# Optimization experiments

Measured on AMD Instinct MI355X. Metric: run time of the kernel, lower is better.

Reference implementation:

```python
import jax, jax.numpy as jnp
import numpy as np

B, E, C = 128, 16, 128   # batch, n experts (program tokens), module_dim
H = W = 64               # input image size
PROJ, FC, NANS = 512, 1024, 2


def conv2d(x, w, b, padding=1):
    # x: [N,C,H,W], w: [O,I,kh,kw]
    y = jax.lax.conv_general_dilated(
        x, w, (1, 1), [(padding, padding), (padding, padding)],
        dimension_numbers=('NCHW', 'OIHW', 'NCHW'))
    return y + b[None, :, None, None]


def maxpool2(x):
    return jax.lax.reduce_window(x, -jnp.inf, jax.lax.max, (1, 1, 2, 2), (1, 1, 2, 2), 'VALID')


def setup_inputs() -> dict:
    key = jax.random.key(0)
    ks = jax.random.split(key, 12)
    def init(k, shape, fan_in):
        return jax.random.normal(k, shape, jnp.float32) * np.float32(1.0 / np.sqrt(fan_in))
    inp = {}
    inp['image'] = jax.random.normal(ks[0], (B, 3, H, W), jnp.float32)
    inp['question'] = jax.random.randint(ks[1], (B, 8), 0, E)
    # stem: conv3x3 3->C, relu, maxpool2, conv3x3 C->C, relu, maxpool2
    inp['stem_w1'] = init(ks[2], (C, 3, 3, 3), 3 * 9)
    inp['stem_b1'] = jnp.zeros((C,), jnp.float32)
    inp['stem_w2'] = init(ks[3], (C, C, 3, 3), C * 9)
    inp['stem_b2'] = jnp.zeros((C,), jnp.float32)
    # E expert residual blocks, each: conv3x3 C->C, relu, conv3x3 C->C, +res, relu
    inp['exp_w1'] = init(ks[4], (E, C, C, 3, 3), C * 9)
    inp['exp_b1'] = jnp.zeros((E, C), jnp.float32)
    inp['exp_w2'] = init(ks[5], (E, C, C, 3, 3), C * 9)
    inp['exp_b2'] = jnp.zeros((E, C), jnp.float32)
    # classifier: 1x1 conv C->PROJ, relu, maxpool2, flatten, fc->FC, relu, fc->NANS
    inp['proj_w'] = init(ks[6], (PROJ, C, 1, 1), C)
    inp['proj_b'] = jnp.zeros((PROJ,), jnp.float32)
    inp['fc1_w'] = init(ks[7], (FC, PROJ * 8 * 8), PROJ * 8 * 8)
    inp['fc1_b'] = jnp.zeros((FC,), jnp.float32)
    inp['fc2_w'] = init(ks[8], (NANS, FC), FC)
    inp['fc2_b'] = jnp.zeros((NANS,), jnp.float32)
    return inp


def reference(image, question, stem_w1, stem_b1, stem_w2, stem_b2,
              exp_w1, exp_b1, exp_w2, exp_b2,
              proj_w, proj_b, fc1_w, fc1_b, fc2_w, fc2_b):
    # stem -> [B, C, 16, 16]
    h = maxpool2(jax.nn.relu(conv2d(image, stem_w1, stem_b1)))
    h = maxpool2(jax.nn.relu(conv2d(h, stem_w2, stem_b2)))

    def block(x, w1, b1, w2, b2):
        # per-sample residual block with per-sample expert weights; x: [C,h,w]
        x4 = x[None]
        out = jax.nn.relu(conv2d(x4, w1, b1))
        out = conv2d(out, w2, b2)
        return jax.nn.relu(x4 + out)[0]

    # dispatch order matches [color_lhs, lhs, color_rhs, rhs, rel] = cols 3,4,6,7,5
    for col in (3, 4, 6, 7, 5):
        idx = question[:, col]
        h = jax.vmap(block)(h, exp_w1[idx], exp_b1[idx], exp_w2[idx], exp_b2[idx])

    # classifier
    p = maxpool2(jax.nn.relu(conv2d(h, proj_w, proj_b, padding=0)))  # [B,PROJ,8,8]
    f = p.reshape(p.shape[0], -1)
    f = jax.nn.relu(f @ fc1_w.T + fc1_b)
    return f @ fc2_w.T + fc2_b
```

## Files before the change

### kernel.cpp

```cpp
#include <hip/hip_runtime.h>
#include <hip/hip_bf16.h>
#include <cstdint>
#include <cstddef>


typedef __bf16 bf16_t;
typedef __attribute__((ext_vector_type(4))) bf16_t bf16x4;
typedef __attribute__((ext_vector_type(8))) bf16_t bf16x8;
typedef __attribute__((ext_vector_type(16))) float f32x16;
typedef __attribute__((ext_vector_type(4))) float f32x4;

__global__ __launch_bounds__(256) void prep_stem1_k(
    const float* __restrict__ exp_w1, const float* __restrict__ exp_w2,
    const float* __restrict__ stem_w2, const float* __restrict__ proj_w,
    bf16_t* __restrict__ wT1, bf16_t* __restrict__ wT2,
    bf16_t* __restrict__ wTs2, bf16_t* __restrict__ pwT,
    const float* __restrict__ img, const float* __restrict__ w1,
    const float* __restrict__ b1, bf16_t* __restrict__ s1out,
    const float* __restrict__ fc1_w, bf16_t* __restrict__ wbf)
{
  alignas(16) __shared__ char smem[37120];
  int bid = blockIdx.x;
  const int tid = threadIdx.x;

  if (bid >= 2376) {
    const size_t base0 = (size_t)(bid - 2376) * 16384 + (size_t)tid * 8;
#pragma unroll
    for (int it = 0; it < 8; ++it) {
      const size_t idx = base0 + (size_t)it * 2048;
      f32x4 u0 = *(const f32x4*)(fc1_w + idx);
      f32x4 u1 = *(const f32x4*)(fc1_w + idx + 4);
      bf16x8 v;
#pragma unroll
      for (int j = 0; j < 4; ++j) { v[j] = (bf16_t)u0[j]; v[4 + j] = (bf16_t)u1[j]; }
      *(bf16x8*)(wbf + idx) = v;
    }
    return;
  }

  if (bid >= 328) {
    bid -= 328;
    float* sImg = (float*)smem;
    char*  sOut = smem + 4112;
    const int b = bid >> 4, t = bid & 15;
    const int ty0p = (t >> 2) * 8, tx0p = (t & 3) * 8;
    const int lane = tid & 63;
    const int wvbase = __builtin_amdgcn_readfirstlane(tid >> 6) * 32;

    for (int s = tid; s < 972; s += 256) {
      const int ic = s / 324, r2 = s - ic * 324;
      const int rr = r2 / 18, cc = r2 - rr * 18;
      const int gy = 2 * ty0p - 1 + rr, gx = 2 * tx0p - 1 + cc;
      float v = 0.f;
      if (gy >= 0 && gy < 64 && gx >= 0 && gx < 64)
        v = img[(((size_t)b * 3 + ic) * 64 + gy) * 64 + gx];
      sImg[ic * 342 + rr * 19 + cc] = v;
    }
    __syncthreads();

    const int ppy = lane >> 3, ppx = lane & 7;
    const int swz = (lane & 15) << 3;
    char* orow = sOut + lane * 256;

    for (int oc8 = 0; oc8 < 32; oc8 += 8) {
      float acc[8][2][2];
#pragma unroll
      for (int q = 0; q < 8; ++q) {
        const float bv = b1[wvbase + oc8 + q];
#pragma unroll
        for (int i = 0; i < 2; ++i)
#pragma unroll
          for (int jj = 0; jj < 2; ++jj) acc[q][i][jj] = bv;
      }
#pragma unroll
      for (int ic = 0; ic < 3; ++ic)
#pragma unroll
        for (int dy = 0; dy < 3; ++dy)
#pragma unroll
          for (int dx = 0; dx < 3; ++dx) {
            const float p00 = sImg[ic * 342 + (2 * ppy + dy) * 19 + 2 * ppx + dx];
            const float p01 = sImg[ic * 342 + (2 * ppy + dy) * 19 + 2 * ppx + dx + 1];
            const float p10 = sImg[ic * 342 + (2 * ppy + dy + 1) * 19 + 2 * ppx + dx];
            const float p11 = sImg[ic * 342 + (2 * ppy + dy + 1) * 19 + 2 * ppx + dx + 1];
#pragma unroll
            for (int q = 0; q < 8; ++q) {
              const float wv2 = w1[(wvbase + oc8 + q) * 27 + ic * 9 + dy * 3 + dx];
              acc[q][0][0] = fmaf(p00, wv2, acc[q][0][0]);
              acc[q][0][1] = fmaf(p01, wv2, acc[q][0][1]);
              acc[q][1][0] = fmaf(p10, wv2, acc[q][1][0]);
              acc[q][1][1] = fmaf(p11, wv2, acc[q][1][1]);
            }
          }
#pragma unroll
      for (int h4 = 0; h4 < 8; h4 += 4) {
        bf16x4 qv;
#pragma unroll
        for (int j = 0; j < 4; ++j) {
          const int q = h4 + j;
          const float mx = fmaxf(fmaxf(acc[q][0][0], acc[q][0][1]),
                                 fmaxf(acc[q][1][0], acc[q][1][1]));
          qv[j] = (bf16_t)fmaxf(mx, 0.f);
        }
        *(bf16x4*)(orow + (((wvbase + oc8 + h4) * 2) ^ swz)) = qv;
      }
    }
    __syncthreads();

#pragma unroll
    for (int it = 0; it < 4; ++it) {
      const int idx = it * 256 + tid;
      const int px = idx >> 4, ch8 = idx & 15;
      const int sw = (px & 15) << 3;
      const char* rb = sOut + px * 256;
      bf16x4 lo = *(const bf16x4*)(rb + ((ch8 * 16) ^ sw));
      bf16x4 hi = *(const bf16x4*)(rb + ((ch8 * 16 + 8) ^ sw));
      bf16x8 v;
#pragma unroll
      for (int j = 0; j < 4; ++j) { v[j] = lo[j]; v[4 + j] = hi[j]; }
      const int gpy = ty0p + (px >> 3), gpx = tx0p + (px & 7);
      *(bf16x8*)(s1out + ((size_t)(b * 1024 + gpy * 32 + gpx)) * 128 + ch8 * 8) = v;
    }
    return;
  }

  if (bid >= 264) {
    const int base = (bid - 264) * 1024 + tid;
#pragma unroll
    for (int it = 0; it < 4; ++it) {
      const int idx = base + it * 256;
      const int oc = idx >> 7, ic = idx & 127;
      const int og = oc >> 5, cc2 = oc & 31;
      const int ich2 = ic >> 6, icl = ic & 63;
      const int kh2 = icl >> 4, g2 = (icl >> 3) & 1, j2 = icl & 7;
      const int off = ((((og * 2 + ich2) * 4 + kh2) << 9)) + ((g2 << 5) + cc2) * 8 + j2;
      pwT[off] = (bf16_t)proj_w[(size_t)oc * 128 + ic];
    }
    return;
  }

  const float* in;
  bf16_t* out;
  if (bid < 128)      { in = exp_w1;  out = wT1; }
  else if (bid < 256) { in = exp_w2;  out = wT2;  bid -= 128; }
  else                { in = stem_w2; out = wTs2; bid -= 256; }
  const int e   = bid >> 3;
  const int rem = bid & 7;
  const int ocg = rem >> 1, ich = rem & 1;

  float* sW = (float*)smem;
  bf16_t* outb = out + (size_t)e * 147456;

  for (int h = 0; h < 2; ++h) {
    if (h) __syncthreads();
    for (int idx = tid; idx < 2304; idx += 256) {
      const int r16 = idx / 144, q = idx - r16 * 144;
      const float* src = in + (size_t)(e * 128 + ocg * 32 + h * 16 + r16) * 1152
                       + ich * 576 + q * 4;
      *(f32x4*)(&sW[r16 * 580 + q * 4]) = *(const f32x4*)src;
    }
    __syncthreads();
    for (int c = tid; c < 1152; c += 256) {
      const int dd  = c >> 7;
      const int kh  = (c >> 5) & 3;
      const int g2  = (c >> 4) & 1;
      const int c16 = c & 15;
      const int cc  = h * 16 + c16;
      bf16x8 v;
#pragma unroll
      for (int j = 0; j < 8; ++j)
        v[j] = (bf16_t)sW[c16 * 580 + (kh * 16 + g2 * 8 + j) * 9 + dd];
      bf16_t* op = outb + ((size_t)(((ocg * 2 + ich) * 9 + dd) * 4 + kh) << 9)
                 + (g2 * 32 + cc) * 8;
      *(bf16x8*)op = v;
    }
  }
}

__global__ __launch_bounds__(256) void conv_stem2_k(
    const bf16_t* __restrict__ act, const bf16_t* __restrict__ wF,
    const float* __restrict__ bias, bf16_t* __restrict__ out)
{
  const int b = blockIdx.x >> 4, ph = blockIdx.x & 15;
  const int y0 = ph * 2;
  const int tid = threadIdx.x, lane = tid & 63, wv = tid >> 6;
  const int g = lane >> 5, cc = lane & 31;
  const int wq = wv;

  __shared__ bf16_t simg[272 * 64];

  f32x16 acc[2];
#pragma unroll
  for (int i = 0; i < 2; ++i)
#pragma unroll
    for (int r = 0; r < 16; ++r) acc[i][r] = 0.f;

  const bf16_t* wfb = wF + ((size_t)(wq * 2) * 9 * 4 << 9) + lane * 8;

  for (int p = tid; p < 272; p += 256) {
    const int ich = p / 136, r2 = p - ich * 136;
    const int yy = r2 / 34, xx = r2 - yy * 34;
    const int gy = y0 + yy - 1, gx = xx - 1;
    const bool inb = (gy >= 0 && gy < 32 && gx >= 0 && gx < 32);
    const bf16_t* src = act + ((size_t)(b * 1024 + gy * 32 + gx)) * 128 + ich * 64;
#pragma unroll
    for (int j = 0; j < 8; ++j) {
      bf16x8 v = {};
      if (inb) v = *(const bf16x8*)(src + j * 8);
      const int waddr = (p * 128 + j * 16) ^ ((p & 7) << 4);
      *(bf16x8*)((char*)simg + waddr) = v;
    }
  }
  __syncthreads();

#pragma unroll
  for (int ich = 0; ich < 2; ++ich) {
#pragma unroll
    for (int dydx = 0; dydx < 9; ++dydx) {
      const int dy = dydx / 3, dx = dydx - dy * 3;
      const bf16_t* wf = wfb + (((ich * 9 + dydx) * 4) << 9);
#pragma unroll
      for (int kh = 0; kh < 4; ++kh) {
        const bf16x8 a = *(const bf16x8*)(wf + (kh << 9));
#pragma unroll
        for (int r = 0; r < 2; ++r) {
          const int s = ich * 136 + (r + dy) * 34 + cc + dx;
          const int raddr = (s * 128 + (kh * 2 + g) * 16) ^ ((s & 7) << 4);
          const bf16x8 bbv = *(const bf16x8*)((const char*)simg + raddr);
          acc[r] = __builtin_amdgcn_mfma_f32_32x32x16_bf16(a, bbv, acc[r], 0, 0, 0);
        }
      }
    }
  }

  const int pxp = cc >> 1;
  bf16_t* op = out + ((size_t)(b * 256 + ph * 16 + pxp)) * 128;
#pragma unroll
  for (int rq = 0; rq < 4; ++rq) {
    const int oc4 = wq * 32 + rq * 8 + g * 4;
    const f32x4 bi = *(const f32x4*)(bias + oc4);
    bf16x4 qv;
#pragma unroll
    for (int j = 0; j < 4; ++j) {
      const int r = rq * 4 + j;
      float v = fmaxf(acc[0][r], acc[1][r]);
      v = fmaxf(v, __shfl_xor(v, 1));
      qv[j] = (bf16_t)fmaxf(v + bi[j], 0.f);
    }
    if ((cc & 1) == 0) *(bf16x4*)(op + oc4) = qv;
  }
}

template<int RES>
__global__ __launch_bounds__(256) void conv_exp_k(
    const bf16_t* __restrict__ act, const bf16_t* __restrict__ wF,
    const float* __restrict__ bias, const int* __restrict__ question, int col,
    const bf16_t* __restrict__ res, bf16_t* __restrict__ out)
{
  const int b = blockIdx.x >> 2, ph = blockIdx.x & 3;
  const int y0 = ph * 4;
  const int e = question[b * 8 + col];
  const int tid = threadIdx.x, lane = tid & 63, wv = tid >> 6;
  const int g = lane >> 5, cc = lane & 31;
  const int wq_oc = wv & 1, wq_px = wv >> 1;

  __shared__ bf16_t simg[216 * 64];

  f32x16 acc[2];
#pragma unroll
  for (int i = 0; i < 2; ++i)
#pragma unroll
    for (int r = 0; r < 16; ++r) acc[i][r] = 0.f;

  const int px = wq_px * 32 + cc;
  const int sl = (px >> 4) * 18 + (px & 15);

  const bf16_t* wfb = wF + (size_t)e * 147456
                    + (((size_t)(wq_oc * 2) * 2) * 9 * 4 << 9) + lane * 8;

  for (int p = tid; p < 216; p += 256) {
    const int ich = p / 108, r2 = p - ich * 108;
    const int yy = r2 / 18, xx = r2 - yy * 18;
    const int gy = y0 + yy - 1, gx = xx - 1;
    const bool inb = (gy >= 0 && gy < 16 && gx >= 0 && gx < 16);
    const bf16_t* src = act + ((size_t)(b * 256 + gy * 16 + gx)) * 128 + ich * 64;
#pragma unroll
    for (int j = 0; j < 8; ++j) {
      bf16x8 v = {};
      if (inb) v = *(const bf16x8*)(src + j * 8);
      const int waddr = (p * 128 + j * 16) ^ ((p & 7) << 4);
      *(bf16x8*)((char*)simg + waddr) = v;
    }
  }
  __syncthreads();

#pragma unroll
  for (int ich = 0; ich < 2; ++ich) {
#pragma unroll
    for (int dydx = 0; dydx < 9; ++dydx) {
      const int dy = dydx / 3, dx = dydx - dy * 3;
      const int sbase = ich * 108 + sl + dy * 18 + dx;
      const bf16_t* wf = wfb + (((ich * 9 + dydx) * 4) << 9);
#pragma unroll
      for (int kh = 0; kh < 4; ++kh) {
        const bf16x8 a0 = *(const bf16x8*)(wf + (kh << 9));
        const bf16x8 a1 = *(const bf16x8*)(wf + 36864 + (kh << 9));
        const int raddr = (sbase * 128 + (kh * 2 + g) * 16) ^ ((sbase & 7) << 4);
        const bf16x8 bbv = *(const bf16x8*)((const char*)simg + raddr);
        acc[0] = __builtin_amdgcn_mfma_f32_32x32x16_bf16(a0, bbv, acc[0], 0, 0, 0);
        acc[1] = __builtin_amdgcn_mfma_f32_32x32x16_bf16(a1, bbv, acc[1], 0, 0, 0);
      }
    }
  }

  const float* bb = bias + e * 128;
  const size_t pixbase = ((size_t)(b * 256 + (y0 + (px >> 4)) * 16 + (px & 15))) * 128;
  bf16_t* op = out + pixbase;
#pragma unroll
  for (int mf = 0; mf < 2; ++mf) {
#pragma unroll
    for (int rq = 0; rq < 4; ++rq) {
      const int oc4 = wq_oc * 64 + mf * 32 + rq * 8 + g * 4;
      const f32x4 bi = *(const f32x4*)(bb + oc4);
      bf16x4 qv;
      bf16x4 rv = {};
      if (RES) rv = *(const bf16x4*)(res + pixbase + oc4);
#pragma unroll
      for (int j = 0; j < 4; ++j) {
        float v = acc[mf][rq * 4 + j] + bi[j];
        if (RES) v += (float)rv[j];
        qv[j] = (bf16_t)fmaxf(v, 0.f);
      }
      *(bf16x4*)(op + oc4) = qv;
    }
  }
}

__global__ __launch_bounds__(256) void proj_mfma_k(
    const bf16_t* __restrict__ h, const bf16_t* __restrict__ pwF,
    const float* __restrict__ pb, bf16_t* __restrict__ f)
{
  const int b = blockIdx.x >> 2, ocg = blockIdx.x & 3;
  const int tid = threadIdx.x, lane = tid & 63, wv = tid >> 6;
  const int g = lane >> 5, cc = lane & 31;
  const int wq_oc = wv & 1, wq_px = wv >> 1;

  __shared__ bf16_t simg[256 * 64];

  f32x16 acc[2][4];
#pragma unroll
  for (int i = 0; i < 2; ++i)
#pragma unroll
    for (int j = 0; j < 4; ++j)
#pragma unroll
      for (int r = 0; r < 16; ++r) acc[i][j][r] = 0.f;

  const int px0 = wq_px * 128 + cc;
  const int og0 = ocg * 4 + wq_oc * 2;
  const bf16_t* pfb = pwF + (((size_t)og0 * 2 * 4) << 9) + lane * 8;

  for (int ich = 0; ich < 2; ++ich) {
    __syncthreads();
    {
      const int p = tid;
      const bf16_t* src = h + ((size_t)(b * 256 + p)) * 128 + ich * 64;
#pragma unroll
      for (int j = 0; j < 8; ++j) {
        bf16x8 v = *(const bf16x8*)(src + j * 8);
        const int waddr = (p * 128 + j * 16) ^ ((p & 7) << 4);
        *(bf16x8*)((char*)simg + waddr) = v;
      }
    }
    __syncthreads();

#pragma unroll
    for (int kh = 0; kh < 4; ++kh) {
      const bf16x8 a0 = *(const bf16x8*)(pfb + ((ich * 4 + kh) << 9));
      const bf16x8 a1 = *(const bf16x8*)(pfb + 4096 + ((ich * 4 + kh) << 9));
#pragma unroll
      for (int nf = 0; nf < 4; ++nf) {
        const int s = px0 + nf * 32;
        const int raddr = (s * 128 + (kh * 2 + g) * 16) ^ ((s & 7) << 4);
        const bf16x8 bb = *(const bf16x8*)((const char*)simg + raddr);
        acc[0][nf] = __builtin_amdgcn_mfma_f32_32x32x16_bf16(a0, bb, acc[0][nf], 0, 0, 0);
        acc[1][nf] = __builtin_amdgcn_mfma_f32_32x32x16_bf16(a1, bb, acc[1][nf], 0, 0, 0);
      }
    }
  }

#pragma unroll
  for (int mf = 0; mf < 2; ++mf) {
#pragma unroll
    for (int nf = 0; nf < 4; ++nf) {
      const int px = px0 + nf * 32;
      const int x = px & 15;
      const int py = wq_px * 4 + nf;
      const int pxp = x >> 1;
#pragma unroll
      for (int r = 0; r < 16; ++r) {
        float v = acc[mf][nf][r];
        v = fmaxf(v, __shfl_xor(v, 1));
        v = fmaxf(v, __shfl_xor(v, 16));
        const int oc = ocg * 128 + wq_oc * 64 + mf * 32 + (r & 3) + 8 * (r >> 2) + 4 * g;
        v = fmaxf(v + pb[oc], 0.f);
        if ((cc & 17) == 0)
          f[((size_t)(b * 512 + oc)) * 64 + py * 8 + pxp] = (bf16_t)v;
      }
    }
  }
}

__global__ __launch_bounds__(256) void fc1_mfma_k(
    const bf16_t* __restrict__ A, const bf16_t* __restrict__ Wb,
    float* __restrict__ part)
{
  const int nt = blockIdx.x;
  const int ks = blockIdx.y;
  const int n0 = nt * 64;
  const int k0 = ks * 1024;
  const int tid = threadIdx.x, lane = tid & 63, wv = tid >> 6;
  const int g = lane >> 5, cc = lane & 31;
  const int mh = wv & 1, nh = wv >> 1;

  __shared__ char sA[16384];
  __shared__ char sB[8192];

  f32x16 acc0, acc1;
#pragma unroll
  for (int r = 0; r < 16; ++r) { acc0[r] = 0.f; acc1[r] = 0.f; }

  for (int t = 0; t < 16; ++t) {
    __syncthreads();
#pragma unroll
    for (int i = 0; i < 4; ++i) {
      const int c = tid + i * 256;
      const int row = c >> 3, ko = c & 7;
      bf16x8 v = *(const bf16x8*)(A + (size_t)row * 32768 + k0 + t * 64 + ko * 8);
      const int wa = (row * 128 + ko * 16) ^ ((row & 7) << 4);
      *(bf16x8*)(sA + wa) = v;
    }
#pragma unroll
    for (int i = 0; i < 2; ++i) {
      const int c = tid + i * 256;
      const int row = c >> 3, ko = c & 7;
      bf16x8 v = *(const bf16x8*)(Wb + (size_t)(n0 + row) * 32768 + k0 + t * 64 + ko * 8);
      const int wa = (row * 128 + ko * 16) ^ ((row & 7) << 4);
      *(bf16x8*)(sB + wa) = v;
    }
    __syncthreads();
#pragma unroll
    for (int kss = 0; kss < 4; ++kss) {
      const int kb = kss * 32 + g * 16;
      const int rA0 = mh * 64 + cc, rA1 = rA0 + 32;
      const bf16x8 a0 = *(const bf16x8*)(sA + ((rA0 * 128 + kb) ^ ((rA0 & 7) << 4)));
      const bf16x8 a1 = *(const bf16x8*)(sA + ((rA1 * 128 + kb) ^ ((rA1 & 7) << 4)));
      const int rB = nh * 32 + cc;
      const bf16x8 bb = *(const bf16x8*)(sB + ((rB * 128 + kb) ^ ((rB & 7) << 4)));
      acc0 = __builtin_amdgcn_mfma_f32_32x32x16_bf16(a0, bb, acc0, 0, 0, 0);
      acc1 = __builtin_amdgcn_mfma_f32_32x32x16_bf16(a1, bb, acc1, 0, 0, 0);
    }
  }

  float* pp = part + ((size_t)ks * 128) * 1024 + n0 + nh * 32 + cc;
#pragma unroll
  for (int r = 0; r < 16; ++r) {
    const int m0 = mh * 64 + (r & 3) + 8 * (r >> 2) + 4 * g;
    pp[(size_t)m0 * 1024] = acc0[r];
    pp[(size_t)(m0 + 32) * 1024] = acc1[r];
  }
}

__global__ __launch_bounds__(256) void fc1_red_k(
    const float* __restrict__ part, const float* __restrict__ bias, float* __restrict__ fo)
{
  const int i = blockIdx.x * 256 + threadIdx.x;
  const int m = i >> 10, j = i & 1023;
  float s = bias[j];
#pragma unroll
  for (int ks = 0; ks < 32; ++ks) s += part[((size_t)ks * 128 + m) * 1024 + j];
  fo[i] = fmaxf(s, 0.f);
}

__global__ __launch_bounds__(256) void fc2_k(
    const float* __restrict__ fo, const float* __restrict__ w2,
    const float* __restrict__ b2, float* __restrict__ out)
{
  const int m = blockIdx.x;
  const int tid = threadIdx.x;
  float a0 = 0.f, a1 = 0.f;
  for (int k = tid; k < 1024; k += 256) {
    const float fv = fo[(size_t)m * 1024 + k];
    a0 = fmaf(fv, w2[k], a0);
    a1 = fmaf(fv, w2[1024 + k], a1);
  }
#pragma unroll
  for (int o = 32; o > 0; o >>= 1) {
    a0 += __shfl_down(a0, o);
    a1 += __shfl_down(a1, o);
  }
  __shared__ float r0[4], r1[4];
  const int wid = tid >> 6;
  if ((tid & 63) == 0) { r0[wid] = a0; r1[wid] = a1; }
  __syncthreads();
  if (tid == 0) {
    out[(size_t)m * 2 + 0] = r0[0] + r0[1] + r0[2] + r0[3] + b2[0];
    out[(size_t)m * 2 + 1] = r1[0] + r1[1] + r1[2] + r1[3] + b2[1];
  }
}

extern "C" void kernel_launch(void* const* d_in, const int* in_sizes, int n_in,
                              void* d_out, int out_size, void* d_ws, size_t ws_size,
                              hipStream_t stream)
{
  const float* image    = (const float*)d_in[0];
  const int*   question = (const int*)  d_in[1];
  const float* stem_w1  = (const float*)d_in[2];
  const float* stem_b1  = (const float*)d_in[3];
  const float* stem_w2  = (const float*)d_in[4];
  const float* stem_b2  = (const float*)d_in[5];
  const float* exp_w1   = (const float*)d_in[6];
  const float* exp_b1   = (const float*)d_in[7];
  const float* exp_w2   = (const float*)d_in[8];
  const float* exp_b2   = (const float*)d_in[9];
  const float* proj_w   = (const float*)d_in[10];
  const float* proj_b   = (const float*)d_in[11];
  const float* fc1_w    = (const float*)d_in[12];
  const float* fc1_b    = (const float*)d_in[13];
  const float* fc2_w    = (const float*)d_in[14];
  const float* fc2_b    = (const float*)d_in[15];
  float* out = (float*)d_out;

  char* base = (char*)d_ws;
  bf16_t* actA   = (bf16_t*)(base + 33554432);
  bf16_t* actH   = (bf16_t*)(base + 67108864);
  bf16_t* actT   = (bf16_t*)(base + 75497472);
  bf16_t* wT1    = (bf16_t*)(base + 83886080);
  bf16_t* wT2    = (bf16_t*)(base + 88604672);
  bf16_t* wTs2   = (bf16_t*)(base + 93323264);
  bf16_t* pwT    = (bf16_t*)(base + 93618176);
  bf16_t* wbf    = (bf16_t*)(base + 93749248);
  bf16_t* fbf  = (bf16_t*)base;
  float*  part = (float*)(base + 8388608);
  float*  f1o  = (float*)(base + 25165824);

  prep_stem1_k<<<4424, 256, 0, stream>>>(exp_w1, exp_w2, stem_w2, proj_w,
                                         wT1, wT2, wTs2, pwT,
                                         image, stem_w1, stem_b1, actA,
                                         fc1_w, wbf);

  conv_stem2_k<<<2048, 256, 0, stream>>>(actA, wTs2, stem_b2, actH);

  const int cols[5] = {3, 4, 6, 7, 5};
  for (int i = 0; i < 5; ++i) {
    conv_exp_k<0><<<512, 256, 0, stream>>>(actH, wT1, exp_b1, question, cols[i],
                                           nullptr, actT);
    conv_exp_k<1><<<512, 256, 0, stream>>>(actT, wT2, exp_b2, question, cols[i],
                                           actH, actH);
  }

  proj_mfma_k<<<512, 256, 0, stream>>>(actH, pwT, proj_b, fbf);
  fc1_mfma_k<<<dim3(16, 32), 256, 0, stream>>>(fbf, wbf, part);
  fc1_red_k<<<512, 256, 0, stream>>>(part, fc1_b, f1o);
  fc2_k<<<128, 256, 0, stream>>>(f1o, fc2_w, fc2_b, out);
}
```

Measured before the change: 362.5 us.

## Spread fc1 weight bf16 conversion across expert conv launches

Moves the fc1_w fp32-to-bf16 conversion blocks out of the prep/stem1 kernel and spreads them as extra blocks across the ten expert conv launches, about 205 blocks each. The expert convs launch only 512 blocks, so the idea is to fill idle CUs with this bandwidth-bound conversion work and shorten the prep kernel. The risk is that the extra conversion blocks compete for memory bandwidth with the conv blocks, and it adds a workgroup-count dependency to every launch.

```diff
diff --git a/kernel.cpp b/kernel.cpp
--- a/kernel.cpp
+++ b/kernel.cpp
@@ -16,27 +16,11 @@
     bf16_t* __restrict__ wT1, bf16_t* __restrict__ wT2,
     bf16_t* __restrict__ wTs2, bf16_t* __restrict__ pwT,
     const float* __restrict__ img, const float* __restrict__ w1,
-    const float* __restrict__ b1, bf16_t* __restrict__ s1out,
-    const float* __restrict__ fc1_w, bf16_t* __restrict__ wbf)
+    const float* __restrict__ b1, bf16_t* __restrict__ s1out)
 {
   alignas(16) __shared__ char smem[37120];
   int bid = blockIdx.x;
   const int tid = threadIdx.x;
-
-  if (bid >= 2376) {
-    const size_t base0 = (size_t)(bid - 2376) * 16384 + (size_t)tid * 8;
-#pragma unroll
-    for (int it = 0; it < 8; ++it) {
-      const size_t idx = base0 + (size_t)it * 2048;
-      f32x4 u0 = *(const f32x4*)(fc1_w + idx);
-      f32x4 u1 = *(const f32x4*)(fc1_w + idx + 4);
-      bf16x8 v;
-#pragma unroll
-      for (int j = 0; j < 4; ++j) { v[j] = (bf16_t)u0[j]; v[4 + j] = (bf16_t)u1[j]; }
-      *(bf16x8*)(wbf + idx) = v;
-    }
-    return;
-  }
 
   if (bid >= 328) {
     bid -= 328;
@@ -254,12 +238,30 @@
 __global__ __launch_bounds__(256) void conv_exp_k(
     const bf16_t* __restrict__ act, const bf16_t* __restrict__ wF,
     const float* __restrict__ bias, const int* __restrict__ question, int col,
-    const bf16_t* __restrict__ res, bf16_t* __restrict__ out)
-{
+    const bf16_t* __restrict__ res, bf16_t* __restrict__ out,
+    const float* __restrict__ fc1_w, bf16_t* __restrict__ wbf, int cvt_base)
+{
+  const int tid = threadIdx.x;
+  if (blockIdx.x >= 512) {
+    const size_t base0 = ((size_t)(cvt_base + (int)blockIdx.x - 512) << 14)
+                       + (size_t)tid * 8;
+#pragma unroll
+    for (int it = 0; it < 8; ++it) {
+      const size_t idx = base0 + (size_t)it * 2048;
+      f32x4 u0 = *(const f32x4*)(fc1_w + idx);
+      f32x4 u1 = *(const f32x4*)(fc1_w + idx + 4);
+      bf16x8 v;
+#pragma unroll
+      for (int j = 0; j < 4; ++j) { v[j] = (bf16_t)u0[j]; v[4 + j] = (bf16_t)u1[j]; }
+      *(bf16x8*)(wbf + idx) = v;
+    }
+    return;
+  }
+
   const int b = blockIdx.x >> 2, ph = blockIdx.x & 3;
   const int y0 = ph * 4;
   const int e = question[b * 8 + col];
-  const int tid = threadIdx.x, lane = tid & 63, wv = tid >> 6;
+  const int lane = tid & 63, wv = tid >> 6;
   const int g = lane >> 5, cc = lane & 31;
   const int wq_oc = wv & 1, wq_px = wv >> 1;
 
@@ -542,19 +544,25 @@
   float*  part = (float*)(base + 8388608);
   float*  f1o  = (float*)(base + 25165824);
 
-  prep_stem1_k<<<4424, 256, 0, stream>>>(exp_w1, exp_w2, stem_w2, proj_w,
+  prep_stem1_k<<<2376, 256, 0, stream>>>(exp_w1, exp_w2, stem_w2, proj_w,
                                          wT1, wT2, wTs2, pwT,
-                                         image, stem_w1, stem_b1, actA,
-                                         fc1_w, wbf);
+                                         image, stem_w1, stem_b1, actA);
 
   conv_stem2_k<<<2048, 256, 0, stream>>>(actA, wTs2, stem_b2, actH);
 
   const int cols[5] = {3, 4, 6, 7, 5};
+  int cvt_base = 0;
   for (int i = 0; i < 5; ++i) {
-    conv_exp_k<0><<<512, 256, 0, stream>>>(actH, wT1, exp_b1, question, cols[i],
-                                           nullptr, actT);
-    conv_exp_k<1><<<512, 256, 0, stream>>>(actT, wT2, exp_b2, question, cols[i],
-                                           actH, actH);
+    const int cnt0 = (2 * i < 8) ? 205 : 204;
+    conv_exp_k<0><<<512 + cnt0, 256, 0, stream>>>(actH, wT1, exp_b1, question,
+                                                  cols[i], nullptr, actT,
+                                                  fc1_w, wbf, cvt_base);
+    cvt_base += cnt0;
+    const int cnt1 = (2 * i + 1 < 8) ? 205 : 204;
+    conv_exp_k<1><<<512 + cnt1, 256, 0, stream>>>(actT, wT2, exp_b2, question,
+                                                  cols[i], actH, actH,
+                                                  fc1_w, wbf, cvt_base);
+    cvt_base += cnt1;
   }
 
   proj_mfma_k<<<512, 256, 0, stream>>>(actH, pwT, proj_b, fbf);
```

Result: slower. 383.5 us (+5.8%).
